# Kernel tuning notes

Measured on AMD Instinct MI355X. Metric: run time of the kernel, lower is better.

Reference implementation:

```python
import jax, jax.numpy as jnp
import numpy as np

ALPHA = 1.5
A = 0.5
BANDWIDTH = 1.0
SPHERE_RADIUS = 1.0
HIDDEN = 1024
HEAD = 64
EPS_ACOS = 1e-07
EPS_NORM = 1e-12  # torch F.normalize clamp_min eps


def _l2norm(v):
    # F.normalize(v, p=2, dim=-1)
    n = jnp.sqrt(jnp.sum(v * v, axis=-1, keepdims=True))
    return v / jnp.maximum(n, EPS_NORM)


def setup_inputs() -> dict:
    key = jax.random.key(0)
    ks = jax.random.split(key, 7)
    B, S = 8, 2048
    s = 1.0 / np.sqrt(HIDDEN)
    return {
        "x": jax.random.normal(ks[0], (B, S, HIDDEN), dtype=jnp.float32),
        "Wq": jax.random.uniform(ks[1], (HIDDEN, HEAD), jnp.float32, -s, s),
        "bq": jax.random.uniform(ks[2], (HEAD,), jnp.float32, -s, s),
        "Wk": jax.random.uniform(ks[3], (HIDDEN, HEAD), jnp.float32, -s, s),
        "bk": jax.random.uniform(ks[4], (HEAD,), jnp.float32, -s, s),
        "Wv": jax.random.uniform(ks[5], (HIDDEN, HEAD), jnp.float32, -s, s),
        "bv": jax.random.uniform(ks[6], (HEAD,), jnp.float32, -s, s),
    }


def reference(x, Wq, bq, Wk, bk, Wv, bv):
    # q,k,v: [B,S,HEAD], L2-normalized along feature axis
    q = _l2norm(jnp.einsum("bsh,hd->bsd", x, Wq) + bq)
    k = _l2norm(jnp.einsum("bsh,hd->bsd", x, Wk) + bk)
    v = _l2norm(jnp.einsum("bsh,hd->bsd", x, Wv) + bv)

    # geodesic distance on sphere: [B,S,S]
    cos = jnp.einsum("bqd,bkd->bqk", q, k)
    g_dist = jnp.arccos(jnp.clip(cos, -1.0 + EPS_ACOS, 1.0 - EPS_ACOS)) * SPHERE_RADIUS

    # alpha < 2 -> power-law score
    score = (1.0 + g_dist / jnp.sqrt(BANDWIDTH)) ** (-HEAD - ALPHA)

    # dual degree normalization (a != 0): diag(row^-a) @ S @ diag(col^-a),
    # expressed as broadcast row/col scaling (same math, no diag_embed matmuls)
    r = jnp.sum(score, axis=-1) ** (-A)  # [B,Sq]
    c = jnp.sum(score, axis=-2) ** (-A)  # [B,Sk]
    k_tilde = r[..., :, None] * score * c[..., None, :]

    # L1 normalize over key axis (F.normalize p=1): entries are positive
    denom = jnp.maximum(jnp.sum(jnp.abs(k_tilde), axis=-1, keepdims=True), EPS_NORM)
    probs = k_tilde / denom

    out = jnp.einsum("bqk,bkd->bqd", probs, v)
    return (out, probs)
```

## Files before the change

kernel.cpp:

```cpp
#include <hip/hip_runtime.h>
#include <hip/hip_bf16.h>
#include <math.h>

#define BB 8
#define SS 2048
#define HH 1024
#define DD 64
#define NCV 65

typedef __attribute__((ext_vector_type(8))) short bf16x8;
typedef __attribute__((ext_vector_type(4))) float f32x4;
typedef __attribute__((ext_vector_type(16))) float f32x16;

#define MFMA16(a, b, c) __builtin_amdgcn_mfma_f32_16x16x32_bf16(a, b, c, 0, 0, 0)
#define MFMA32(a, b, c) __builtin_amdgcn_mfma_f32_32x32x16_bf16(a, b, c, 0, 0, 0)

__device__ __forceinline__ ushort bf16rne(float f) {
    uint u = __float_as_uint(f);
    uint r = (u + 0x7FFFu + ((u >> 16) & 1u)) >> 16;
    return (ushort)r;
}
__device__ __forceinline__ ushort bfc(float f) {
    __hip_bfloat16 h = __float2bfloat16(f);
    return *reinterpret_cast<ushort*>(&h);
}
__device__ __forceinline__ float bf2f(ushort h) {
    return __uint_as_float(((uint)h) << 16);
}

__device__ __forceinline__ float score_fn(float cosv) {
    float ax = fminf(fabsf(cosv), 1.0f - 1e-7f);
    float p = fmaf(ax, -0.0012624911f, 0.0066700901f);
    p = fmaf(ax, p, -0.0170881256f);
    p = fmaf(ax, p, 0.0308918810f);
    p = fmaf(ax, p, -0.0501743046f);
    p = fmaf(ax, p, 0.0889789874f);
    p = fmaf(ax, p, -0.2145988016f);
    p = fmaf(ax, p, 1.5707963050f);
    float r = sqrtf(1.0f - ax) * p;
    float g = (cosv >= 0.0f) ? r : (3.14159265358979f - r);
    return exp2f(-65.5f * log2f(1.0f + g));
}

__global__ __launch_bounds__(256) void k_prep(
    const float* __restrict__ Wq, const float* __restrict__ Wk, const float* __restrict__ Wv,
    const float* __restrict__ bq, const float* __restrict__ bk, const float* __restrict__ bv,
    ushort* __restrict__ Whi, ushort* __restrict__ Wlo, float* __restrict__ bcat)
{
    const int n = blockIdx.x;
    const int m = n >> 6, d = n & 63;
    const float* W = (m == 0) ? Wq : (m == 1 ? Wk : Wv);
    #pragma unroll
    for (int i = 0; i < 4; ++i) {
        int j = i * 256 + threadIdx.x;
        float f = W[(size_t)j * DD + d];
        ushort h = bf16rne(f);
        Whi[(size_t)n * HH + j] = h;
        Wlo[(size_t)n * HH + j] = bf16rne(f - bf2f(h));
    }
    if (n == 0 && threadIdx.x < 192) {
        int t = threadIdx.x, mm = t >> 6, dd = t & 63;
        const float* b = (mm == 0) ? bq : (mm == 1 ? bk : bv);
        bcat[t] = b[dd];
    }
}

__global__ __launch_bounds__(256) void k_projmm(
    const float* __restrict__ x, const ushort* __restrict__ Whi,
    const ushort* __restrict__ Wlo, const float* __restrict__ bcat,
    ushort* __restrict__ qh, ushort* __restrict__ ql,
    ushort* __restrict__ kh, ushort* __restrict__ kl,
    float* __restrict__ vw)
{
    __shared__ __align__(16) char smem[32 * 193 * 4];
    __shared__ float rns[96];
    __shared__ float bsh[192];
    ushort* xhi = (ushort*)smem;
    ushort* xlo = xhi + 32 * 128;
    float* ctile = (float*)smem;

    const int t = threadIdx.x;
    const int lane = t & 63;
    const int wid = t >> 6;
    const int row0 = blockIdx.x * 32;
    if (t < 192) bsh[t] = bcat[t];

    f32x4 acc[2][3];
    #pragma unroll
    for (int ar = 0; ar < 2; ++ar)
        #pragma unroll
        for (int bc = 0; bc < 3; ++bc)
            acc[ar][bc] = (f32x4){0.f, 0.f, 0.f, 0.f};

    for (int ch = 0; ch < 8; ++ch) {
        const int j0 = ch * 128;
        __syncthreads();
        #pragma unroll
        for (int i = 0; i < 2; ++i) {
            int u = i * 256 + t;
            int row = u >> 4, uc = u & 15;
            const float* xp = &x[(size_t)(row0 + row) * HH + j0 + uc * 8];
            float4 a = *(const float4*)xp;
            float4 b = *(const float4*)(xp + 4);
            float fs[8] = {a.x, a.y, a.z, a.w, b.x, b.y, b.z, b.w};
            bf16x8 hv, lv;
            #pragma unroll
            for (int e = 0; e < 8; ++e) {
                ushort h = bf16rne(fs[e]);
                hv[e] = (short)h;
                lv[e] = (short)bf16rne(fs[e] - bf2f(h));
            }
            int su = uc ^ (row & 7);
            *(bf16x8*)(xhi + row * 128 + su * 8) = hv;
            *(bf16x8*)(xlo + row * 128 + su * 8) = lv;
        }
        __syncthreads();
        #pragma unroll
        for (int ks = 0; ks < 4; ++ks) {
            bf16x8 ah[2], al[2], bh[3], bl[3];
            #pragma unroll
            for (int ar = 0; ar < 2; ++ar) {
                int row = ar * 16 + (lane & 15);
                int su = (ks * 4 + (lane >> 4)) ^ (row & 7);
                ah[ar] = *(const bf16x8*)(xhi + row * 128 + su * 8);
                al[ar] = *(const bf16x8*)(xlo + row * 128 + su * 8);
            }
            const int koff = j0 + ks * 32 + (lane >> 4) * 8;
            #pragma unroll
            for (int bc = 0; bc < 3; ++bc) {
                int n = wid * 48 + bc * 16 + (lane & 15);
                bh[bc] = *(const bf16x8*)(Whi + (size_t)n * HH + koff);
                bl[bc] = *(const bf16x8*)(Wlo + (size_t)n * HH + koff);
            }
            #pragma unroll
            for (int ar = 0; ar < 2; ++ar)
                #pragma unroll
                for (int bc = 0; bc < 3; ++bc) {
                    acc[ar][bc] = MFMA16(ah[ar], bh[bc], acc[ar][bc]);
                    acc[ar][bc] = MFMA16(ah[ar], bl[bc], acc[ar][bc]);
                    acc[ar][bc] = MFMA16(al[ar], bh[bc], acc[ar][bc]);
                }
        }
    }
    __syncthreads();
    #pragma unroll
    for (int ar = 0; ar < 2; ++ar)
        #pragma unroll
        for (int bc = 0; bc < 3; ++bc) {
            int n = wid * 48 + bc * 16 + (lane & 15);
            #pragma unroll
            for (int r = 0; r < 4; ++r) {
                int row = ar * 16 + (lane >> 4) * 4 + r;
                ctile[row * 193 + n] = acc[ar][bc][r];
            }
        }
    __syncthreads();
    if (t < 96) {
        int mat = t >> 5, row = t & 31;
        float ss = 0.f;
        #pragma unroll 8
        for (int d = 0; d < 64; ++d) {
            float v = ctile[row * 193 + mat * 64 + d] + bsh[mat * 64 + d];
            ss = fmaf(v, v, ss);
        }
        rns[t] = 1.0f / fmaxf(sqrtf(ss), 1e-12f);
    }
    __syncthreads();
    #pragma unroll
    for (int i = 0; i < 24; ++i) {
        int idx = i * 256 + t;
        int row = idx / 192;
        int n = idx - row * 192;
        float v = (ctile[row * 193 + n] + bsh[n]) * rns[(n >> 6) * 32 + row];
        size_t off = (size_t)(row0 + row) * DD + (n & 63);
        if (n < 64) {
            ushort h = bf16rne(v);
            qh[off] = h; ql[off] = bf16rne(v - bf2f(h));
        } else if (n < 128) {
            ushort h = bf16rne(v);
            kh[off] = h; kl[off] = bf16rne(v - bf2f(h));
        } else {
            vw[off] = v;
        }
    }
}

#define K_LOAD(H0,H1,H2,H3,L0,L1,L2,L3, KT) { \
    const ushort* kp = kh + (size_t)(b * SS + kbase + (KT) * 32 + qrow) * DD + kg; \
    const ushort* lp = kl + (size_t)(b * SS + kbase + (KT) * 32 + qrow) * DD + kg; \
    H0 = *(const bf16x8*)(kp);      L0 = *(const bf16x8*)(lp); \
    H1 = *(const bf16x8*)(kp + 16); L1 = *(const bf16x8*)(lp + 16); \
    H2 = *(const bf16x8*)(kp + 32); L2 = *(const bf16x8*)(lp + 32); \
    H3 = *(const bf16x8*)(kp + 48); L3 = *(const bf16x8*)(lp + 48); }

#define K_COMPUTE(H0,H1,H2,H3,L0,L1,L2,L3, KT) { \
    f32x16 acc = Z16; \
    acc = MFMA32(H0, qbh0, acc); acc = MFMA32(H0, qbl0, acc); acc = MFMA32(L0, qbh0, acc); \
    acc = MFMA32(H1, qbh1, acc); acc = MFMA32(H1, qbl1, acc); acc = MFMA32(L1, qbh1, acc); \
    acc = MFMA32(H2, qbh2, acc); acc = MFMA32(H2, qbl2, acc); acc = MFMA32(L2, qbh2, acc); \
    acc = MFMA32(H3, qbh3, acc); acc = MFMA32(H3, qbl3, acc); acc = MFMA32(L3, qbh3, acc); \
    const int kb = (w * 128 + (KT) * 32) * 2 + hi8; \
    uint2 wv; \
    wv.x = (uint)bfc(score_fn(acc[0]))  | ((uint)bfc(score_fn(acc[1]))  << 16); \
    wv.y = (uint)bfc(score_fn(acc[2]))  | ((uint)bfc(score_fn(acc[3]))  << 16); \
    *(uint2*)(ldsrow + ((kb +  0) ^ swq)) = wv; \
    wv.x = (uint)bfc(score_fn(acc[4]))  | ((uint)bfc(score_fn(acc[5]))  << 16); \
    wv.y = (uint)bfc(score_fn(acc[6]))  | ((uint)bfc(score_fn(acc[7]))  << 16); \
    *(uint2*)(ldsrow + ((kb + 16) ^ swq)) = wv; \
    wv.x = (uint)bfc(score_fn(acc[8]))  | ((uint)bfc(score_fn(acc[9]))  << 16); \
    wv.y = (uint)bfc(score_fn(acc[10])) | ((uint)bfc(score_fn(acc[11])) << 16); \
    *(uint2*)(ldsrow + ((kb + 32) ^ swq)) = wv; \
    wv.x = (uint)bfc(score_fn(acc[12])) | ((uint)bfc(score_fn(acc[13])) << 16); \
    wv.y = (uint)bfc(score_fn(acc[14])) | ((uint)bfc(score_fn(acc[15])) << 16); \
    *(uint2*)(ldsrow + ((kb + 48) ^ swq)) = wv; }

__global__ __launch_bounds__(256, 4) void k_score(
    const ushort* __restrict__ qh, const ushort* __restrict__ ql,
    const ushort* __restrict__ kh, const ushort* __restrict__ kl,
    ushort* __restrict__ scrS, float* __restrict__ colsum)
{
    __shared__ __align__(16) char slds[32 * 1024];
    const int t = threadIdx.x;
    const int lane = t & 63;
    const int w = t >> 6;
    const int bid = blockIdx.x;
    const int b  = bid >> 8;
    const int q0 = ((bid >> 2) & 63) * 32;
    const int kgB = (bid & 3) * 512;
    const int kbase = kgB + w * 128;
    const int qrow = lane & 31;
    const int kg = (lane >> 5) * 8;
    const int hi8 = (lane >> 5) * 8;
    const int swq = (qrow & 15) << 3;
    char* ldsrow = slds + qrow * 1024;
    const f32x16 Z16 = {0.f,0.f,0.f,0.f,0.f,0.f,0.f,0.f,0.f,0.f,0.f,0.f,0.f,0.f,0.f,0.f};

    const size_t qoff = (size_t)(b * SS + q0 + qrow) * DD + kg;
    bf16x8 qbh0 = *(const bf16x8*)(qh + qoff);
    bf16x8 qbh1 = *(const bf16x8*)(qh + qoff + 16);
    bf16x8 qbh2 = *(const bf16x8*)(qh + qoff + 32);
    bf16x8 qbh3 = *(const bf16x8*)(qh + qoff + 48);
    bf16x8 qbl0 = *(const bf16x8*)(ql + qoff);
    bf16x8 qbl1 = *(const bf16x8*)(ql + qoff + 16);
    bf16x8 qbl2 = *(const bf16x8*)(ql + qoff + 32);
    bf16x8 qbl3 = *(const bf16x8*)(ql + qoff + 48);

    bf16x8 xh0, xh1, xh2, xh3, xl0, xl1, xl2, xl3;
    bf16x8 yh0, yh1, yh2, yh3, yl0, yl1, yl2, yl3;
    K_LOAD(xh0,xh1,xh2,xh3,xl0,xl1,xl2,xl3, 0)
    K_LOAD(yh0,yh1,yh2,yh3,yl0,yl1,yl2,yl3, 1)
    K_COMPUTE(xh0,xh1,xh2,xh3,xl0,xl1,xl2,xl3, 0)
    K_LOAD(xh0,xh1,xh2,xh3,xl0,xl1,xl2,xl3, 2)
    K_COMPUTE(yh0,yh1,yh2,yh3,yl0,yl1,yl2,yl3, 1)
    K_LOAD(yh0,yh1,yh2,yh3,yl0,yl1,yl2,yl3, 3)
    K_COMPUTE(xh0,xh1,xh2,xh3,xl0,xl1,xl2,xl3, 2)
    K_COMPUTE(yh0,yh1,yh2,yh3,yl0,yl1,yl2,yl3, 3)

    __syncthreads();
    {
        float s0 = 0.f, s1 = 0.f;
        #pragma unroll 8
        for (int r = 0; r < 32; ++r) {
            uint d = *(const uint*)(slds + r * 1024 + ((t * 4) ^ ((r & 15) << 3)));
            s0 += bf2f((ushort)(d & 0xFFFFu));
            s1 += bf2f((ushort)(d >> 16));
        }
        atomicAdd(&colsum[b * SS + kgB + t * 2 + 0], s0);
        atomicAdd(&colsum[b * SS + kgB + t * 2 + 1], s1);
    }
    {
        const int r = t >> 3;
        const int swr = (r & 15) << 3;
        const char* lrow = slds + r * 1024;
        ushort* srowg = scrS + (size_t)(b * SS + q0 + r) * 4096 + 2048 + kgB;
        #pragma unroll
        for (int i = 0; i < 8; ++i) {
            int c = (t & 7) + i * 8;
            int lc = c * 16;
            uint2 a = *(const uint2*)(lrow + (lc ^ swr));
            uint2 bb = *(const uint2*)(lrow + ((lc + 8) ^ swr));
            uint4 v;
            v.x = a.x; v.y = a.y; v.z = bb.x; v.w = bb.y;
            *(uint4*)(srowg + c * 8) = v;
        }
    }
}

__global__ __launch_bounds__(256) void k_cvc(
    const float* __restrict__ vw, const float* __restrict__ colsum,
    ushort* __restrict__ cvT)
{
    __shared__ float vs[64][65];
    __shared__ float csh[64];
    const int t = threadIdx.x;
    const int b = blockIdx.x >> 5;
    const int k0 = (blockIdx.x & 31) * 64;
    #pragma unroll
    for (int i = 0; i < 4; ++i) {
        int idx = i * 256 + t;
        int r = idx >> 4, c4 = idx & 15;
        float4 v4 = *(const float4*)&vw[(size_t)(b * SS + k0 + r) * DD + c4 * 4];
        *(float4*)&vs[r][c4 * 4] = v4;
    }
    if (t < 64) csh[t] = 1.0f / sqrtf(colsum[b * SS + k0 + t]);
    __syncthreads();
    const int kk4 = (t & 15) * 4;
    #pragma unroll
    for (int jt = 0; jt < 4; ++jt) {
        int j = jt * 16 + (t >> 4);
        uint2 wv;
        wv.x = (uint)bfc(csh[kk4 + 0] * vs[kk4 + 0][j])
             | ((uint)bfc(csh[kk4 + 1] * vs[kk4 + 1][j]) << 16);
        wv.y = (uint)bfc(csh[kk4 + 2] * vs[kk4 + 2][j])
             | ((uint)bfc(csh[kk4 + 3] * vs[kk4 + 3][j]) << 16);
        *(uint2*)(cvT + ((size_t)b * NCV + j) * SS + k0 + kk4) = wv;
    }
    if (t < 16) {
        uint2 wv;
        wv.x = (uint)bfc(csh[t * 4 + 0]) | ((uint)bfc(csh[t * 4 + 1]) << 16);
        wv.y = (uint)bfc(csh[t * 4 + 2]) | ((uint)bfc(csh[t * 4 + 3]) << 16);
        *(uint2*)(cvT + ((size_t)b * NCV + 64) * SS + k0 + t * 4) = wv;
    }
}

__global__ __launch_bounds__(256, 4) void k_ndp(
    const ushort* __restrict__ scrS, const ushort* __restrict__ cvT,
    float* __restrict__ probs, float* __restrict__ out)
{
    __shared__ float nred[16][64];
    __shared__ float dPart[4][16];
    __shared__ float dInv[16];
    const int t = threadIdx.x;
    const int lane = t & 63;
    const int w = t >> 6;
    const int b = blockIdx.x >> 7;
    const int q0 = (blockIdx.x & 127) * 16;
    const int kbase = w * 512;
    const int qn = lane & 15;
    const int g = lane >> 4;

    ((float*)nred)[t] = 0.f; ((float*)nred)[t + 256] = 0.f;
    ((float*)nred)[t + 512] = 0.f; ((float*)nred)[t + 768] = 0.f;
    __syncthreads();

    const ushort* cslice = cvT + (size_t)b * NCV * SS;
    const ushort* cbrow = cslice + (size_t)64 * SS;

    float dacc = 0.f;
    f32x4 nacc[4];
    #pragma unroll
    for (int ct = 0; ct < 4; ++ct) nacc[ct] = (f32x4){0.f, 0.f, 0.f, 0.f};

    const ushort* sp = scrS + (size_t)(b * SS + q0 + qn) * 4096 + 2048 + kbase + g * 8;
    const ushort* cp = cbrow + kbase + g * 8;
    const ushort* p0 = cslice + (size_t)(0 * 16 + qn) * SS + kbase + g * 8;
    const ushort* p1 = cslice + (size_t)(1 * 16 + qn) * SS + kbase + g * 8;
    const ushort* p2 = cslice + (size_t)(2 * 16 + qn) * SS + kbase + g * 8;
    const ushort* p3 = cslice + (size_t)(3 * 16 + qn) * SS + kbase + g * 8;

    #pragma unroll 4
    for (int ch = 0; ch < 16; ++ch) {
        bf16x8 s8 = *(const bf16x8*)sp;
        bf16x8 c8 = *(const bf16x8*)cp;
        bf16x8 b0 = *(const bf16x8*)p0;
        bf16x8 b1 = *(const bf16x8*)p1;
        bf16x8 b2 = *(const bf16x8*)p2;
        bf16x8 b3 = *(const bf16x8*)p3;
        #pragma unroll
        for (int e = 0; e < 8; ++e)
            dacc = fmaf(bf2f((ushort)s8[e]), bf2f((ushort)c8[e]), dacc);
        nacc[0] = MFMA16(s8, b0, nacc[0]);
        nacc[1] = MFMA16(s8, b1, nacc[1]);
        nacc[2] = MFMA16(s8, b2, nacc[2]);
        nacc[3] = MFMA16(s8, b3, nacc[3]);
        sp += 32; cp += 32; p0 += 32; p1 += 32; p2 += 32; p3 += 32;
    }
    {
        float d = dacc;
        d += __shfl_xor(d, 16, 64);
        d += __shfl_xor(d, 32, 64);
        if (lane < 16) dPart[w][lane] = d;
    }
    __syncthreads();
    if (t < 16) dInv[t] = 1.0f / (dPart[0][t] + dPart[1][t] + dPart[2][t] + dPart[3][t]);
    #pragma unroll
    for (int ct = 0; ct < 4; ++ct)
        #pragma unroll
        for (int r = 0; r < 4; ++r)
            atomicAdd(&nred[g * 4 + r][ct * 16 + qn], nacc[ct][r]);
    __syncthreads();
    {
        int q = t >> 4, c4 = (t & 15) * 4;
        float di = dInv[q];
        float4 o;
        o.x = nred[q][c4] * di;     o.y = nred[q][c4 + 1] * di;
        o.z = nred[q][c4 + 2] * di; o.w = nred[q][c4 + 3] * di;
        *(float4*)&out[(size_t)(b * SS + q0 + q) * DD + c4] = o;
    }
    float cf[8];
    {
        bf16x8 c8 = *(const bf16x8*)(cbrow + t * 8);
        #pragma unroll
        for (int e = 0; e < 8; ++e) cf[e] = bf2f((ushort)c8[e]);
    }
    #pragma unroll
    for (int rb = 0; rb < 4; ++rb) {
        bf16x8 s[4];
        float dl[4];
        #pragma unroll
        for (int j = 0; j < 4; ++j) {
            int row = rb * 4 + j;
            s[j] = *(const bf16x8*)(scrS + (size_t)(b * SS + q0 + row) * 4096 + 2048 + t * 8);
            dl[j] = dInv[row];
        }
        __syncthreads();
        #pragma unroll
        for (int j = 0; j < 4; ++j) {
            f32x4 o0, o1;
            o0[0] = bf2f((ushort)s[j][0]) * cf[0] * dl[j];
            o0[1] = bf2f((ushort)s[j][1]) * cf[1] * dl[j];
            o0[2] = bf2f((ushort)s[j][2]) * cf[2] * dl[j];
            o0[3] = bf2f((ushort)s[j][3]) * cf[3] * dl[j];
            o1[0] = bf2f((ushort)s[j][4]) * cf[4] * dl[j];
            o1[1] = bf2f((ushort)s[j][5]) * cf[5] * dl[j];
            o1[2] = bf2f((ushort)s[j][6]) * cf[6] * dl[j];
            o1[3] = bf2f((ushort)s[j][7]) * cf[7] * dl[j];
            float* prow = probs + (size_t)(b * SS + q0 + rb * 4 + j) * SS + t * 8;
            __builtin_nontemporal_store(o0, (f32x4*)prow);
            __builtin_nontemporal_store(o1, (f32x4*)(prow + 4));
        }
    }
}

extern "C" void kernel_launch(void* const* d_in, const int* in_sizes, int n_in,
                              void* d_out, int out_size, void* d_ws, size_t ws_size,
                              hipStream_t stream)
{
    const float* x  = (const float*)d_in[0];
    const float* Wq = (const float*)d_in[1];
    const float* bq = (const float*)d_in[2];
    const float* Wk = (const float*)d_in[3];
    const float* bk = (const float*)d_in[4];
    const float* Wv = (const float*)d_in[5];
    const float* bv = (const float*)d_in[6];

    float* out   = (float*)d_out;
    float* probs = out + (size_t)BB * SS * DD;
    ushort* scrS = (ushort*)probs;

    const size_t NQ = (size_t)BB * SS * DD;
    ushort* qh    = (ushort*)d_ws;
    ushort* ql    = qh + NQ;
    ushort* kh    = ql + NQ;
    ushort* kl    = kh + NQ;
    float*  vw    = (float*)(kl + NQ);
    float*  colsum = vw + NQ;
    ushort* cvT   = (ushort*)(colsum + BB * SS);
    ushort* Whi   = cvT + (size_t)BB * NCV * SS;
    ushort* Wlo   = Whi + (size_t)192 * HH;
    float*  bcat  = (float*)(Wlo + (size_t)192 * HH);

    hipMemsetAsync(colsum, 0, BB * SS * sizeof(float), stream);
    k_prep  <<<192, 256, 0, stream>>>(Wq, Wk, Wv, bq, bk, bv, Whi, Wlo, bcat);
    k_projmm<<<512, 256, 0, stream>>>(x, Whi, Wlo, bcat, qh, ql, kh, kl, vw);
    k_score <<<2048, 256, 0, stream>>>(qh, ql, kh, kl, scrS, colsum);
    k_cvc   <<<256, 256, 0, stream>>>(vw, colsum, cvT);
    k_ndp   <<<1024, 256, 0, stream>>>(scrS, cvT, probs, out);
}
```

Baseline: 191.1 us.

## Split normalization kernel into separate output and probs-writing kernels

```diff
diff --git a/kernel.cpp b/kernel.cpp
--- a/kernel.cpp
+++ b/kernel.cpp
@@ -323,9 +323,9 @@
     }
 }
 
-__global__ __launch_bounds__(256, 4) void k_ndp(
+__global__ __launch_bounds__(256, 4) void k_nd(
     const ushort* __restrict__ scrS, const ushort* __restrict__ cvT,
-    float* __restrict__ probs, float* __restrict__ out)
+    float* __restrict__ dinv_g, float* __restrict__ out)
 {
     __shared__ float nred[16][64];
     __shared__ float dPart[4][16];
@@ -382,7 +382,11 @@
         if (lane < 16) dPart[w][lane] = d;
     }
     __syncthreads();
-    if (t < 16) dInv[t] = 1.0f / (dPart[0][t] + dPart[1][t] + dPart[2][t] + dPart[3][t]);
+    if (t < 16) {
+        float di = 1.0f / (dPart[0][t] + dPart[1][t] + dPart[2][t] + dPart[3][t]);
+        dInv[t] = di;
+        dinv_g[b * SS + q0 + t] = di;
+    }
     #pragma unroll
     for (int ct = 0; ct < 4; ++ct)
         #pragma unroll
@@ -397,38 +401,45 @@
         o.z = nred[q][c4 + 2] * di; o.w = nred[q][c4 + 3] * di;
         *(float4*)&out[(size_t)(b * SS + q0 + q) * DD + c4] = o;
     }
+}
+
+__global__ __launch_bounds__(256) void k_probs(
+    const ushort* __restrict__ scrS, const ushort* __restrict__ cvT,
+    const float* __restrict__ dinv_g, float* __restrict__ probs)
+{
+    const int t = threadIdx.x;
+    const int b = blockIdx.x >> 9;
+    const int r0 = (blockIdx.x & 511) * 4;
+    const ushort* cbrow = cvT + ((size_t)b * NCV + 64) * SS;
+
     float cf[8];
     {
         bf16x8 c8 = *(const bf16x8*)(cbrow + t * 8);
         #pragma unroll
         for (int e = 0; e < 8; ++e) cf[e] = bf2f((ushort)c8[e]);
     }
-    #pragma unroll
-    for (int rb = 0; rb < 4; ++rb) {
-        bf16x8 s[4];
-        float dl[4];
-        #pragma unroll
-        for (int j = 0; j < 4; ++j) {
-            int row = rb * 4 + j;
-            s[j] = *(const bf16x8*)(scrS + (size_t)(b * SS + q0 + row) * 4096 + 2048 + t * 8);
-            dl[j] = dInv[row];
-        }
-        __syncthreads();
-        #pragma unroll
-        for (int j = 0; j < 4; ++j) {
-            f32x4 o0, o1;
-            o0[0] = bf2f((ushort)s[j][0]) * cf[0] * dl[j];
-            o0[1] = bf2f((ushort)s[j][1]) * cf[1] * dl[j];
-            o0[2] = bf2f((ushort)s[j][2]) * cf[2] * dl[j];
-            o0[3] = bf2f((ushort)s[j][3]) * cf[3] * dl[j];
-            o1[0] = bf2f((ushort)s[j][4]) * cf[4] * dl[j];
-            o1[1] = bf2f((ushort)s[j][5]) * cf[5] * dl[j];
-            o1[2] = bf2f((ushort)s[j][6]) * cf[6] * dl[j];
-            o1[3] = bf2f((ushort)s[j][7]) * cf[7] * dl[j];
-            float* prow = probs + (size_t)(b * SS + q0 + rb * 4 + j) * SS + t * 8;
-            __builtin_nontemporal_store(o0, (f32x4*)prow);
-            __builtin_nontemporal_store(o1, (f32x4*)(prow + 4));
-        }
+    bf16x8 s[4];
+    float dl[4];
+    #pragma unroll
+    for (int j = 0; j < 4; ++j) {
+        s[j] = *(const bf16x8*)(scrS + (size_t)(b * SS + r0 + j) * 4096 + 2048 + t * 8);
+        dl[j] = dinv_g[b * SS + r0 + j];
+    }
+    __syncthreads();
+    #pragma unroll
+    for (int j = 0; j < 4; ++j) {
+        f32x4 o0, o1;
+        o0[0] = bf2f((ushort)s[j][0]) * cf[0] * dl[j];
+        o0[1] = bf2f((ushort)s[j][1]) * cf[1] * dl[j];
+        o0[2] = bf2f((ushort)s[j][2]) * cf[2] * dl[j];
+        o0[3] = bf2f((ushort)s[j][3]) * cf[3] * dl[j];
+        o1[0] = bf2f((ushort)s[j][4]) * cf[4] * dl[j];
+        o1[1] = bf2f((ushort)s[j][5]) * cf[5] * dl[j];
+        o1[2] = bf2f((ushort)s[j][6]) * cf[6] * dl[j];
+        o1[3] = bf2f((ushort)s[j][7]) * cf[7] * dl[j];
+        float* prow = probs + (size_t)(b * SS + r0 + j) * SS + t * 8;
+        __builtin_nontemporal_store(o0, (f32x4*)prow);
+        __builtin_nontemporal_store(o1, (f32x4*)(prow + 4));
     }
 }
 
@@ -455,7 +466,8 @@
     ushort* kl    = kh + NQ;
     float*  vw    = (float*)(kl + NQ);
     float*  colsum = vw + NQ;
-    ushort* cvT   = (ushort*)(colsum + BB * SS);
+    float*  dinv  = colsum + BB * SS;
+    ushort* cvT   = (ushort*)(dinv + BB * SS);
     ushort* Whi   = cvT + (size_t)BB * NCV * SS;
     ushort* Wlo   = Whi + (size_t)192 * HH;
     float*  bcat  = (float*)(Wlo + (size_t)192 * HH);
@@ -465,5 +477,6 @@
     k_projmm<<<512, 256, 0, stream>>>(x, Whi, Wlo, bcat, qh, ql, kh, kl, vw);
     k_score <<<2048, 256, 0, stream>>>(qh, ql, kh, kl, scrS, colsum);
     k_cvc   <<<256, 256, 0, stream>>>(vw, colsum, cvT);
-    k_ndp   <<<1024, 256, 0, stream>>>(scrS, cvT, probs, out);
-}
+    k_nd    <<<1024, 256, 0, stream>>>(scrS, cvT, dinv, out);
+    k_probs <<<4096, 256, 0, stream>>>(scrS, cvT, dinv, probs);
+}
```

New measurement: 210.5 us. +10.1%, slower.
